# Performance work log

Measured on AMD Instinct MI355X. Metric: run time of the kernel, lower is better.

## Reference

```python
import jax, jax.numpy as jnp
import numpy as np

F = 26          # field_size
D = 16          # embed_dim
B = 16384       # batch
VOCABS = [1000] * F
OFFSETS = np.concatenate([[0], np.cumsum(VOCABS)[:-1]]).astype(np.int32)
IU, JU = np.triu_indices(F, k=1)   # 325 pairs (i<j)
P = IU.shape[0]
BN_EPS = 1e-3   # Keras BatchNormalization default epsilon


def setup_inputs() -> dict:
    key = jax.random.key(0)
    ks = jax.random.split(key, 8)
    s = 0.05  # keras 'random_normal' initializer stddev
    return {
        "x": jax.random.randint(ks[0], (B, F), 0, 1000, dtype=jnp.int32),
        "emb_table": jax.random.normal(ks[1], (sum(VOCABS) + 1, D), jnp.float32) * s,
        "se_w1": jax.random.normal(ks[2], (F, F // 2), jnp.float32) * s,
        "se_w2": jax.random.normal(ks[3], (F // 2, F), jnp.float32) * s,
        "bl_w": jax.random.normal(ks[4], (P, D, D), jnp.float32) * s,
        "w1": jax.random.normal(ks[5], (F * (F - 1) * D, 64), jnp.float32) * s,
        "b1": jnp.zeros((64,), jnp.float32),
        "g1": jnp.ones((64,), jnp.float32),
        "be1": jnp.zeros((64,), jnp.float32),
        "m1": jnp.zeros((64,), jnp.float32),
        "v1": jnp.ones((64,), jnp.float32),
        "w2": jax.random.normal(ks[6], (64, 32), jnp.float32) * s,
        "b2": jnp.zeros((32,), jnp.float32),
        "g2": jnp.ones((32,), jnp.float32),
        "be2": jnp.zeros((32,), jnp.float32),
        "m2": jnp.zeros((32,), jnp.float32),
        "v2": jnp.ones((32,), jnp.float32),
        "w3": jax.random.normal(ks[7], (32, 1), jnp.float32) * s,
        "b3": jnp.zeros((1,), jnp.float32),
    }


def _bilinear(v, bl_w):
    # v: [B, F, D]; shared W stack over the 325 ordered pairs (i<j)
    # tmp[p] = (v_i @ W_p) * v_j  -> [B, P, D]
    return jnp.einsum('bpd,pde->bpe', v[:, IU], bl_w) * v[:, JU]


def _bn(h, g, b, m, v):
    return g * (h - m) * jax.lax.rsqrt(v + BN_EPS) + b


def reference(x, emb_table, se_w1, se_w2, bl_w,
              w1, b1, g1, be1, m1, v1,
              w2, b2, g2, be2, m2, v2,
              w3, b3):
    ids = x + jnp.asarray(OFFSETS)
    e = emb_table[ids]                         # [B, F, D]
    # SE layer: mean-pool over embed dim, two ReLU dense layers, rescale
    z = e.mean(axis=-1)                        # [B, F]
    A = jax.nn.relu(jax.nn.relu(z @ se_w1) @ se_w2)
    se = e * A[..., None]                      # [B, F, D]
    # Bilinear interaction (same weights for both calls)
    p = _bilinear(e, bl_w).reshape(e.shape[0], -1)     # [B, P*D]
    se_p = _bilinear(se, bl_w).reshape(e.shape[0], -1)
    h = jnp.concatenate([p, se_p], axis=-1)    # [B, F*(F-1)*D]
    # MLP with inference-mode BatchNorm; dropout=0 is a no-op
    h = jax.nn.relu(_bn(h @ w1 + b1, g1, be1, m1, v1))
    h = jax.nn.relu(_bn(h @ w2 + b2, g2, be2, m2, v2))
    return jax.nn.sigmoid(h @ w3 + b3)         # [B, 1]
```

## Files before the change

### kernel.cpp

```cpp
#include <hip/hip_runtime.h>
#include <cstdint>
#include <cstddef>


#define F_FIELDS 26
#define P_PAIRS 325
#define PAD_PAIRS 336
#define BATCH 16384
#define BN_EPS 1e-3f
#define ROWS 64

typedef short bf16x8 __attribute__((ext_vector_type(8)));
typedef float f32x4 __attribute__((ext_vector_type(4)));

struct PairTab { unsigned char iu[PAD_PAIRS]; unsigned char ju[PAD_PAIRS]; };
static constexpr PairTab make_pairs() {
    PairTab t{};
    int p = 0;
    for (int a = 0; a < F_FIELDS; ++a)
        for (int b = a + 1; b < F_FIELDS; ++b) { t.iu[p] = (unsigned char)a; t.ju[p] = (unsigned char)b; ++p; }
    for (; p < PAD_PAIRS; ++p) { t.iu[p] = 0; t.ju[p] = 0; }
    return t;
}
__constant__ PairTab PT = make_pairs();

__device__ __forceinline__ unsigned short bf16u(float v) {
    unsigned u = __float_as_uint(v);
    unsigned r = (u + 0x7fffu + ((u >> 16) & 1u)) >> 16;
    return (unsigned short)r;
}
__device__ __forceinline__ unsigned pk_bf16(float lo, float hi) {
    return (unsigned)bf16u(lo) | ((unsigned)bf16u(hi) << 16);
}
__device__ __forceinline__ float bflo(unsigned d) { return __uint_as_float(d << 16); }
__device__ __forceinline__ float bfhi(unsigned d) { return __uint_as_float(d & 0xffff0000u); }
__device__ __forceinline__ unsigned pk_trunc(float u, float cu) {
    return __builtin_amdgcn_perm(__float_as_uint(cu), __float_as_uint(u), 0x07060302u);
}

__global__ __launch_bounds__(256) void k_wprep(const float* __restrict__ w1,
        const float* __restrict__ blw, unsigned short* __restrict__ w1catL,
        unsigned short* __restrict__ wcatL) {
    const int p = blockIdx.x;
    const int tid = threadIdx.x;
    if (p >= P_PAIRS) {
        int4 z = make_int4(0, 0, 0, 0);
        *(int4*)(w1catL + (size_t)p * 2048 + tid * 8) = z;
        if (tid < 64) *(int4*)(wcatL + (size_t)p * 512 + tid * 8) = z;
        return;
    }
    __shared__ float wu[1024], wv[1024], wb[256];
    ((float4*)wu)[tid] = ((const float4*)(w1 + (size_t)p * 1024))[tid];
    ((float4*)wv)[tid] = ((const float4*)(w1 + 332800 + (size_t)p * 1024))[tid];
    if (tid < 64) ((float4*)wb)[tid] = ((const float4*)(blw + (size_t)p * 256))[tid];
    __syncthreads();
    {
        int nt = tid >> 6, lane = tid & 63, ln = lane & 15, q = lane >> 4;
        int o = nt * 16 + ln;
        unsigned short outv[8];
        #pragma unroll
        for (int j = 0; j < 8; ++j) {
            int k = q * 8 + j, d = k >> 1, su = k & 1;
            outv[j] = bf16u(su ? wv[d * 64 + o] : wu[d * 64 + o]);
        }
        *(int4*)(w1catL + (size_t)p * 2048 + tid * 8) = *(const int4*)outv;
    }
    if (tid < 64) {
        int ln = tid & 15, q = tid >> 4;
        unsigned short outv[8];
        #pragma unroll
        for (int j = 0; j < 8; ++j) {
            int din = q * 8 + j;
            outv[j] = (din < 16) ? bf16u(wb[din * 16 + ln]) : (unsigned short)0;
        }
        *(int4*)(wcatL + (size_t)p * 512 + tid * 8) = *(const int4*)outv;
    }
}

union __align__(16) SMem {
    struct {
        unsigned short eS[ROWS * 424];
        float aS[F_FIELDS * ROWS];
    } a;
    struct {
        unsigned ysh[8 * 8 * 64 * 4];
        float h1s[ROWS * 65];
        float h2s[ROWS * 36];
    } b;
};

__global__ __launch_bounds__(512, 2) void k_main(const int* __restrict__ x,
        const float* __restrict__ emb, const float* __restrict__ sw1,
        const float* __restrict__ sw2, const unsigned short* __restrict__ w1catL,
        const unsigned short* __restrict__ wcatL,
        const float* __restrict__ b1, const float* __restrict__ g1,
        const float* __restrict__ be1, const float* __restrict__ m1,
        const float* __restrict__ v1,
        const float* __restrict__ w2, const float* __restrict__ b2,
        const float* __restrict__ g2, const float* __restrict__ be2,
        const float* __restrict__ m2, const float* __restrict__ v2,
        const float* __restrict__ w3, const float* __restrict__ b3,
        float* __restrict__ out) {
    __shared__ SMem sm;
    __shared__ float z_s[ROWS][F_FIELDS];
    __shared__ float sw1_s[F_FIELDS * 13];
    __shared__ float sw2_s[13 * F_FIELDS];
    const int tid = threadIdx.x;
    const int b0 = blockIdx.x * ROWS;
    unsigned short* eS = sm.a.eS;
    float* aS = sm.a.aS;

    for (int i = tid; i < F_FIELDS * 13; i += 512) { sw1_s[i] = sw1[i]; sw2_s[i] = sw2[i]; }
    for (int idx = tid; idx < ROWS * F_FIELDS; idx += 512) {
        int r = idx / F_FIELDS, f = idx - r * F_FIELDS;
        int id = x[(b0 + r) * F_FIELDS + f] + f * 1000;
        const float4* src = (const float4*)(emb + (size_t)id * 16);
        float4 v0 = src[0], v1l = src[1], v2l = src[2], v3l = src[3];
        int4 o0, o1;
        o0.x = (int)pk_bf16(v0.x, v0.y);  o0.y = (int)pk_bf16(v0.z, v0.w);
        o0.z = (int)pk_bf16(v1l.x, v1l.y); o0.w = (int)pk_bf16(v1l.z, v1l.w);
        o1.x = (int)pk_bf16(v2l.x, v2l.y); o1.y = (int)pk_bf16(v2l.z, v2l.w);
        o1.z = (int)pk_bf16(v3l.x, v3l.y); o1.w = (int)pk_bf16(v3l.z, v3l.w);
        *(int4*)(eS + r * 424 + f * 16) = o0;
        *(int4*)(eS + r * 424 + f * 16 + 8) = o1;
        float s = v0.x + v0.y + v0.z + v0.w + v1l.x + v1l.y + v1l.z + v1l.w
                + v2l.x + v2l.y + v2l.z + v2l.w + v3l.x + v3l.y + v3l.z + v3l.w;
        z_s[r][f] = s * (1.0f / 16.0f);
    }
    __syncthreads();
    if (tid < ROWS) {
        float s1[13];
        #pragma unroll
        for (int o = 0; o < 13; ++o) {
            float acc0 = 0.f;
            #pragma unroll
            for (int f = 0; f < F_FIELDS; ++f) acc0 = fmaf(z_s[tid][f], sw1_s[f * 13 + o], acc0);
            s1[o] = fmaxf(acc0, 0.0f);
        }
        #pragma unroll
        for (int f = 0; f < F_FIELDS; ++f) {
            float acc0 = 0.f;
            #pragma unroll
            for (int o = 0; o < 13; ++o) acc0 = fmaf(s1[o], sw2_s[o * F_FIELDS + f], acc0);
            aS[f * ROWS + tid] = fmaxf(acc0, 0.0f);
        }
    }
    __syncthreads();

    const int w    = __builtin_amdgcn_readfirstlane(tid >> 6);
    const int lane = tid & 63;
    const int ln   = lane & 15;
    const int q    = lane >> 4;
    const int p0 = w * 42, p1 = p0 + 42;

    f32x4 acc[4][4];
    #pragma unroll
    for (int a = 0; a < 4; ++a)
        #pragma unroll
        for (int b = 0; b < 4; ++b) acc[a][b] = (f32x4){0.f, 0.f, 0.f, 0.f};
    const f32x4 zero4 = {0.f, 0.f, 0.f, 0.f};

    int iu_c = PT.iu[p0];
    int ju_c = PT.ju[p0];
    bf16x8 eiB[4];
    float ai[4];
    #pragma unroll
    for (int mt = 0; mt < 4; ++mt) {
        eiB[mt] = __builtin_bit_cast(bf16x8,
            *(const int4*)(eS + (mt * 16 + ln) * 424 + iu_c * 16 + (q & 1) * 8));
        ai[mt] = aS[iu_c * ROWS + mt * 16 + ln];
    }
    bf16x8 wa_c = __builtin_bit_cast(bf16x8, *(const int4*)(wcatL + (size_t)p0 * 512 + lane * 8));
    bf16x8 wb_c[4];
    #pragma unroll
    for (int nt = 0; nt < 4; ++nt)
        wb_c[nt] = __builtin_bit_cast(bf16x8, *(const int4*)(w1catL + (size_t)p0 * 2048 + nt * 512 + lane * 8));
    f32x4 tc[4];
    #pragma unroll
    for (int mt = 0; mt < 4; ++mt)
        tc[mt] = __builtin_amdgcn_mfma_f32_16x16x32_bf16(wa_c, eiB[mt], zero4, 0, 0, 0);

    #pragma unroll 2
    for (int p = p0; p < p1; ++p) {
        const int pn = (p + 1 < p1) ? (p + 1) : p;
        bf16x8 wa_n = __builtin_bit_cast(bf16x8, *(const int4*)(wcatL + (size_t)pn * 512 + lane * 8));
        bf16x8 wb_n[4];
        #pragma unroll
        for (int nt = 0; nt < 4; ++nt)
            wb_n[nt] = __builtin_bit_cast(bf16x8, *(const int4*)(w1catL + (size_t)pn * 2048 + nt * 512 + lane * 8));

        const int ju = ju_c;
        uint2 ejv[4];
        float cv[4];
        #pragma unroll
        for (int mt = 0; mt < 4; ++mt) {
            ejv[mt] = *(const uint2*)(eS + (mt * 16 + ln) * 424 + ju * 16 + q * 4);
            cv[mt]  = ai[mt] * aS[ju * ROWS + mt * 16 + ln];
        }

        const int iu_prev = iu_c;
        ++ju_c;
        if (ju_c == F_FIELDS) {
            ++iu_c;
            if (iu_c >= F_FIELDS - 1) iu_c = 0;
            ju_c = iu_c + 1;
        }
        if (iu_c != iu_prev) {
            #pragma unroll
            for (int mt = 0; mt < 4; ++mt) {
                eiB[mt] = __builtin_bit_cast(bf16x8,
                    *(const int4*)(eS + (mt * 16 + ln) * 424 + iu_c * 16 + (q & 1) * 8));
                ai[mt] = aS[iu_c * ROWS + mt * 16 + ln];
            }
        }

        __builtin_amdgcn_s_setprio(1);
        #pragma unroll
        for (int mt = 0; mt < 4; ++mt) {
            f32x4 t = tc[mt];
            float e0 = bflo(ejv[mt].x), e1 = bfhi(ejv[mt].x);
            float e2 = bflo(ejv[mt].y), e3 = bfhi(ejv[mt].y);
            float c  = cv[mt];
            float u0 = t[0] * e0, u1 = t[1] * e1, u2 = t[2] * e2, u3 = t[3] * e3;
            int4 af;
            af.x = (int)pk_trunc(u0, c * u0);
            af.y = (int)pk_trunc(u1, c * u1);
            af.z = (int)pk_trunc(u2, c * u2);
            af.w = (int)pk_trunc(u3, c * u3);
            bf16x8 A = __builtin_bit_cast(bf16x8, af);
            #pragma unroll
            for (int nt = 0; nt < 4; ++nt)
                acc[mt][nt] = __builtin_amdgcn_mfma_f32_16x16x32_bf16(A, wb_c[nt], acc[mt][nt], 0, 0, 0);
        }
        #pragma unroll
        for (int mt = 0; mt < 4; ++mt)
            tc[mt] = __builtin_amdgcn_mfma_f32_16x16x32_bf16(wa_n, eiB[mt], zero4, 0, 0, 0);
        __builtin_amdgcn_s_setprio(0);
        wa_c = wa_n;
        #pragma unroll
        for (int nt = 0; nt < 4; ++nt) wb_c[nt] = wb_n[nt];
    }

    __syncthreads();
    unsigned* ysh = sm.b.ysh;
    float* h1s = sm.b.h1s;
    float* h2s = sm.b.h2s;
    #pragma unroll
    for (int mt = 0; mt < 4; ++mt)
        #pragma unroll
        for (int nh = 0; nh < 2; ++nh) {
            int nt0 = nh * 2, nt1 = nh * 2 + 1;
            int4 v;
            v.x = (int)pk_bf16(acc[mt][nt0][0], acc[mt][nt0][1]);
            v.y = (int)pk_bf16(acc[mt][nt0][2], acc[mt][nt0][3]);
            v.z = (int)pk_bf16(acc[mt][nt1][0], acc[mt][nt1][1]);
            v.w = (int)pk_bf16(acc[mt][nt1][2], acc[mt][nt1][3]);
            *(int4*)(ysh + ((w * 8 + mt * 2 + nh) * 64 + lane) * 4) = v;
        }
    __syncthreads();

    {
        const int s = tid >> 6, lane2 = tid & 63, ln2 = lane2 & 15, q2 = lane2 >> 4;
        const int mt = s >> 1, nh = s & 1;
        const int c0 = nh * 32 + ln2, c1 = c0 + 16;
        const float sc0 = g1[c0] * rsqrtf(v1[c0] + BN_EPS);
        const float of0 = be1[c0] + sc0 * (b1[c0] - m1[c0]);
        const float sc1 = g1[c1] * rsqrtf(v1[c1] + BN_EPS);
        const float of1 = be1[c1] + sc1 * (b1[c1] - m1[c1]);
        float s8[8];
        #pragma unroll
        for (int i = 0; i < 8; ++i) s8[i] = 0.f;
        #pragma unroll
        for (int wv = 0; wv < 8; ++wv) {
            int4 v = *(const int4*)(ysh + ((wv * 8 + s) * 64 + lane2) * 4);
            s8[0] += bflo((unsigned)v.x); s8[1] += bfhi((unsigned)v.x);
            s8[2] += bflo((unsigned)v.y); s8[3] += bfhi((unsigned)v.y);
            s8[4] += bflo((unsigned)v.z); s8[5] += bfhi((unsigned)v.z);
            s8[6] += bflo((unsigned)v.w); s8[7] += bfhi((unsigned)v.w);
        }
        const int row0 = mt * 16 + q2 * 4;
        #pragma unroll
        for (int r = 0; r < 4; ++r) {
            h1s[(row0 + r) * 65 + c0] = fmaxf(s8[r] * sc0 + of0, 0.f);
            h1s[(row0 + r) * 65 + c1] = fmaxf(s8[4 + r] * sc1 + of1, 0.f);
        }
    }
    __syncthreads();

    {
        const int row = tid >> 3, gg = tid & 7;
        const int o0 = gg * 4;
        float a0 = 0.f, a1 = 0.f, a2 = 0.f, a3 = 0.f;
        #pragma unroll 8
        for (int k = 0; k < 64; ++k) {
            float hk = h1s[row * 65 + k];
            float4 wv = *(const float4*)(w2 + k * 32 + o0);
            a0 = fmaf(hk, wv.x, a0);
            a1 = fmaf(hk, wv.y, a1);
            a2 = fmaf(hk, wv.z, a2);
            a3 = fmaf(hk, wv.w, a3);
        }
        const float4 g2v  = *(const float4*)(g2 + o0);
        const float4 b2v  = *(const float4*)(b2 + o0);
        const float4 m2v  = *(const float4*)(m2 + o0);
        const float4 v2v  = *(const float4*)(v2 + o0);
        const float4 be2v = *(const float4*)(be2 + o0);
        float4 hv;
        hv.x = fmaxf(g2v.x * (a0 + b2v.x - m2v.x) * rsqrtf(v2v.x + BN_EPS) + be2v.x, 0.f);
        hv.y = fmaxf(g2v.y * (a1 + b2v.y - m2v.y) * rsqrtf(v2v.y + BN_EPS) + be2v.y, 0.f);
        hv.z = fmaxf(g2v.z * (a2 + b2v.z - m2v.z) * rsqrtf(v2v.z + BN_EPS) + be2v.z, 0.f);
        hv.w = fmaxf(g2v.w * (a3 + b2v.w - m2v.w) * rsqrtf(v2v.w + BN_EPS) + be2v.w, 0.f);
        *(float4*)(h2s + row * 36 + o0) = hv;
    }
    __syncthreads();
    if (tid < ROWS) {
        float sacc = b3[0];
        #pragma unroll
        for (int k = 0; k < 32; ++k) sacc = fmaf(h2s[tid * 36 + k], w3[k], sacc);
        out[b0 + tid] = 1.0f / (1.0f + expf(-sacc));
    }
}

extern "C" void kernel_launch(void* const* d_in, const int* in_sizes, int n_in,
                              void* d_out, int out_size, void* d_ws, size_t ws_size,
                              hipStream_t stream) {
    const int*   x   = (const int*)d_in[0];
    const float* emb = (const float*)d_in[1];
    const float* sw1 = (const float*)d_in[2];
    const float* sw2 = (const float*)d_in[3];
    const float* blw = (const float*)d_in[4];
    const float* w1  = (const float*)d_in[5];
    const float* b1  = (const float*)d_in[6];
    const float* g1  = (const float*)d_in[7];
    const float* be1 = (const float*)d_in[8];
    const float* m1  = (const float*)d_in[9];
    const float* v1  = (const float*)d_in[10];
    const float* w2  = (const float*)d_in[11];
    const float* b2  = (const float*)d_in[12];
    const float* g2  = (const float*)d_in[13];
    const float* be2 = (const float*)d_in[14];
    const float* m2  = (const float*)d_in[15];
    const float* v2  = (const float*)d_in[16];
    const float* w3  = (const float*)d_in[17];
    const float* b3  = (const float*)d_in[18];
    float* out = (float*)d_out;

    char* ws = (char*)d_ws;
    unsigned short* w1catL = (unsigned short*)ws;
    unsigned short* wcatL  = (unsigned short*)(ws + 1376256);

    hipLaunchKernelGGL(k_wprep, dim3(PAD_PAIRS), dim3(256), 0, stream, w1, blw, w1catL, wcatL);
    hipLaunchKernelGGL(k_main,  dim3(BATCH / ROWS), dim3(512), 0, stream,
                       x, emb, sw1, sw2, w1catL, wcatL,
                       b1, g1, be1, m1, v1, w2, b2, g2, be2, m2, v2, w3, b3, out);
}
```

Baseline: 133.3 us.

## Deepen software pipeline so glue VALU overlaps with accumulation MFMAs

Restructures the per-pair loop into a deeper software pipeline. The first bilinear MFMA now runs two pairs ahead, and the bf16 glue operand for the next pair is built while the current pair's 16 accumulation MFMAs are in flight. The W1 weight prefetch moves one iteration further ahead. The aim is to hide the VALU conversion work and the dependent MFMA latency behind matrix-core work, at the cost of more live registers (A_cur, wb_n, tc) and possible occupancy or spill pressure.

```diff
diff --git a/kernel.cpp b/kernel.cpp
--- a/kernel.cpp
+++ b/kernel.cpp
@@ -160,6 +160,24 @@
         for (int b = 0; b < 4; ++b) acc[a][b] = (f32x4){0.f, 0.f, 0.f, 0.f};
     const f32x4 zero4 = {0.f, 0.f, 0.f, 0.f};
 
+    auto glue = [&](const f32x4* t, const uint2* ejv, const float* cv,
+                    bf16x8* A) {
+        #pragma unroll
+        for (int mt = 0; mt < 4; ++mt) {
+            float e0 = bflo(ejv[mt].x), e1 = bfhi(ejv[mt].x);
+            float e2 = bflo(ejv[mt].y), e3 = bfhi(ejv[mt].y);
+            float c  = cv[mt];
+            float u0 = t[mt][0] * e0, u1 = t[mt][1] * e1;
+            float u2 = t[mt][2] * e2, u3 = t[mt][3] * e3;
+            int4 af;
+            af.x = (int)pk_trunc(u0, c * u0);
+            af.y = (int)pk_trunc(u1, c * u1);
+            af.z = (int)pk_trunc(u2, c * u2);
+            af.w = (int)pk_trunc(u3, c * u3);
+            A[mt] = __builtin_bit_cast(bf16x8, af);
+        }
+    };
+
     int iu_c = PT.iu[p0];
     int ju_c = PT.ju[p0];
     bf16x8 eiB[4];
@@ -170,41 +188,31 @@
             *(const int4*)(eS + (mt * 16 + ln) * 424 + iu_c * 16 + (q & 1) * 8));
         ai[mt] = aS[iu_c * ROWS + mt * 16 + ln];
     }
-    bf16x8 wa_c = __builtin_bit_cast(bf16x8, *(const int4*)(wcatL + (size_t)p0 * 512 + lane * 8));
-    bf16x8 wb_c[4];
+    bf16x8 wb_c[4], wb_n[4];
     #pragma unroll
     for (int nt = 0; nt < 4; ++nt)
         wb_c[nt] = __builtin_bit_cast(bf16x8, *(const int4*)(w1catL + (size_t)p0 * 2048 + nt * 512 + lane * 8));
     f32x4 tc[4];
-    #pragma unroll
-    for (int mt = 0; mt < 4; ++mt)
-        tc[mt] = __builtin_amdgcn_mfma_f32_16x16x32_bf16(wa_c, eiB[mt], zero4, 0, 0, 0);
-
-    #pragma unroll 2
-    for (int p = p0; p < p1; ++p) {
-        const int pn = (p + 1 < p1) ? (p + 1) : p;
-        bf16x8 wa_n = __builtin_bit_cast(bf16x8, *(const int4*)(wcatL + (size_t)pn * 512 + lane * 8));
-        bf16x8 wb_n[4];
-        #pragma unroll
-        for (int nt = 0; nt < 4; ++nt)
-            wb_n[nt] = __builtin_bit_cast(bf16x8, *(const int4*)(w1catL + (size_t)pn * 2048 + nt * 512 + lane * 8));
-
-        const int ju = ju_c;
-        uint2 ejv[4];
-        float cv[4];
+    {
+        bf16x8 wa0 = __builtin_bit_cast(bf16x8, *(const int4*)(wcatL + (size_t)p0 * 512 + lane * 8));
+        #pragma unroll
+        for (int mt = 0; mt < 4; ++mt)
+            tc[mt] = __builtin_amdgcn_mfma_f32_16x16x32_bf16(wa0, eiB[mt], zero4, 0, 0, 0);
+    }
+    bf16x8 A_cur[4];
+    {
+        uint2 ejv[4]; float cv[4];
         #pragma unroll
         for (int mt = 0; mt < 4; ++mt) {
-            ejv[mt] = *(const uint2*)(eS + (mt * 16 + ln) * 424 + ju * 16 + q * 4);
-            cv[mt]  = ai[mt] * aS[ju * ROWS + mt * 16 + ln];
-        }
-
+            ejv[mt] = *(const uint2*)(eS + (mt * 16 + ln) * 424 + ju_c * 16 + q * 4);
+            cv[mt]  = ai[mt] * aS[ju_c * ROWS + mt * 16 + ln];
+        }
+        glue(tc, ejv, cv, A_cur);
+    }
+    {
         const int iu_prev = iu_c;
         ++ju_c;
-        if (ju_c == F_FIELDS) {
-            ++iu_c;
-            if (iu_c >= F_FIELDS - 1) iu_c = 0;
-            ju_c = iu_c + 1;
-        }
+        if (ju_c == F_FIELDS) { ++iu_c; if (iu_c >= F_FIELDS - 1) iu_c = 0; ju_c = iu_c + 1; }
         if (iu_c != iu_prev) {
             #pragma unroll
             for (int mt = 0; mt < 4; ++mt) {
@@ -213,32 +221,65 @@
                 ai[mt] = aS[iu_c * ROWS + mt * 16 + ln];
             }
         }
+    }
+    {
+        const int pn = (p0 + 1 < p1) ? (p0 + 1) : (p1 - 1);
+        bf16x8 wa1 = __builtin_bit_cast(bf16x8, *(const int4*)(wcatL + (size_t)pn * 512 + lane * 8));
+        #pragma unroll
+        for (int nt = 0; nt < 4; ++nt)
+            wb_n[nt] = __builtin_bit_cast(bf16x8, *(const int4*)(w1catL + (size_t)pn * 2048 + nt * 512 + lane * 8));
+        #pragma unroll
+        for (int mt = 0; mt < 4; ++mt)
+            tc[mt] = __builtin_amdgcn_mfma_f32_16x16x32_bf16(wa1, eiB[mt], zero4, 0, 0, 0);
+    }
+
+    #pragma unroll 2
+    for (int p = p0; p < p1; ++p) {
+        const int pn2 = (p + 2 < p1) ? (p + 2) : (p1 - 1);
 
         __builtin_amdgcn_s_setprio(1);
         #pragma unroll
-        for (int mt = 0; mt < 4; ++mt) {
-            f32x4 t = tc[mt];
-            float e0 = bflo(ejv[mt].x), e1 = bfhi(ejv[mt].x);
-            float e2 = bflo(ejv[mt].y), e3 = bfhi(ejv[mt].y);
-            float c  = cv[mt];
-            float u0 = t[0] * e0, u1 = t[1] * e1, u2 = t[2] * e2, u3 = t[3] * e3;
-            int4 af;
-            af.x = (int)pk_trunc(u0, c * u0);
-            af.y = (int)pk_trunc(u1, c * u1);
-            af.z = (int)pk_trunc(u2, c * u2);
-            af.w = (int)pk_trunc(u3, c * u3);
-            bf16x8 A = __builtin_bit_cast(bf16x8, af);
+        for (int mt = 0; mt < 4; ++mt)
             #pragma unroll
             for (int nt = 0; nt < 4; ++nt)
-                acc[mt][nt] = __builtin_amdgcn_mfma_f32_16x16x32_bf16(A, wb_c[nt], acc[mt][nt], 0, 0, 0);
-        }
-        #pragma unroll
-        for (int mt = 0; mt < 4; ++mt)
-            tc[mt] = __builtin_amdgcn_mfma_f32_16x16x32_bf16(wa_n, eiB[mt], zero4, 0, 0, 0);
+                acc[mt][nt] = __builtin_amdgcn_mfma_f32_16x16x32_bf16(A_cur[mt], wb_c[nt], acc[mt][nt], 0, 0, 0);
         __builtin_amdgcn_s_setprio(0);
-        wa_c = wa_n;
+
+        {
+            uint2 ejv[4]; float cv[4];
+            #pragma unroll
+            for (int mt = 0; mt < 4; ++mt) {
+                ejv[mt] = *(const uint2*)(eS + (mt * 16 + ln) * 424 + ju_c * 16 + q * 4);
+                cv[mt]  = ai[mt] * aS[ju_c * ROWS + mt * 16 + ln];
+            }
+            glue(tc, ejv, cv, A_cur);
+        }
+
+        {
+            const int iu_prev = iu_c;
+            ++ju_c;
+            if (ju_c == F_FIELDS) { ++iu_c; if (iu_c >= F_FIELDS - 1) iu_c = 0; ju_c = iu_c + 1; }
+            if (iu_c != iu_prev) {
+                #pragma unroll
+                for (int mt = 0; mt < 4; ++mt) {
+                    eiB[mt] = __builtin_bit_cast(bf16x8,
+                        *(const int4*)(eS + (mt * 16 + ln) * 424 + iu_c * 16 + (q & 1) * 8));
+                    ai[mt] = aS[iu_c * ROWS + mt * 16 + ln];
+                }
+            }
+        }
+
+        {
+            bf16x8 wa2 = __builtin_bit_cast(bf16x8, *(const int4*)(wcatL + (size_t)pn2 * 512 + lane * 8));
+            #pragma unroll
+            for (int mt = 0; mt < 4; ++mt)
+                tc[mt] = __builtin_amdgcn_mfma_f32_16x16x32_bf16(wa2, eiB[mt], zero4, 0, 0, 0);
+        }
         #pragma unroll
         for (int nt = 0; nt < 4; ++nt) wb_c[nt] = wb_n[nt];
+        #pragma unroll
+        for (int nt = 0; nt < 4; ++nt)
+            wb_n[nt] = __builtin_bit_cast(bf16x8, *(const int4*)(w1catL + (size_t)pn2 * 2048 + nt * 512 + lane * 8));
     }
 
     __syncthreads();
```

New measurement: 134.6 us. No clear change (+1.0%).
